# Optimization experiments

Measured on AMD Instinct MI355X. Metric: run time of the kernel, lower is better.

The kernel has to match this reference:

```python
import jax, jax.numpy as jnp
import numpy as np

N_NODES = 50000
N_EDGES = 800000
N_GRAPHS = 2000
N_PAIRS = 4096
IN_CH = 64
EMB = 128
HID = 256
OUT = 1


def gcn_conv(x, edge_index, W, b):
    # PyG GCNConv: h = x @ W^T, then D^{-1/2}(A+I)D^{-1/2} h + b
    h = x @ W.T                                  # [N, out]
    row, col = edge_index[0], edge_index[1]
    ones = jnp.ones((edge_index.shape[1],), h.dtype)
    deg = jax.ops.segment_sum(ones, col, num_segments=N_NODES) + 1.0  # self-loop
    dinv = jax.lax.rsqrt(deg)
    norm = dinv[row] * dinv[col]                 # [E]
    agg = jax.ops.segment_sum(h[row] * norm[:, None], col, num_segments=N_NODES)
    agg = agg + h * (1.0 / deg)[:, None]         # self-loop term (dinv[i]^2)
    return agg + b


def setup_inputs() -> dict:
    key = jax.random.key(0)
    ks = jax.random.split(key, 10)
    x = jax.random.normal(ks[0], (N_NODES, IN_CH), jnp.float32)
    edge_index = jax.random.randint(ks[1], (2, N_EDGES), 0, N_NODES, jnp.int64)
    batch = jnp.sort(jax.random.randint(ks[2], (N_NODES,), 0, N_GRAPHS, jnp.int64))
    drug_drug_batch = jax.random.randint(ks[3], (2, N_PAIRS), 0, N_GRAPHS, jnp.int64)

    def xavier(k, shape):
        fan_out, fan_in = shape
        lim = jnp.sqrt(6.0 / (fan_in + fan_out))
        return jax.random.uniform(k, shape, jnp.float32, -lim, lim)

    return {
        "x": x, "edge_index": edge_index, "batch": batch,
        "drug_drug_batch": drug_drug_batch,
        "conv1_w": xavier(ks[4], (EMB, IN_CH)), "conv1_b": jnp.zeros((EMB,), jnp.float32),
        "conv2_w": xavier(ks[5], (EMB, EMB)), "conv2_b": jnp.zeros((EMB,), jnp.float32),
        "reg1_w": xavier(ks[6], (HID, 2 * EMB)), "reg1_b": jnp.zeros((HID,), jnp.float32),
        "reg2_w": xavier(ks[7], (OUT, HID)), "reg2_b": jnp.zeros((OUT,), jnp.float32),
    }


def reference(x, edge_index, batch, drug_drug_batch,
              conv1_w, conv1_b, conv2_w, conv2_b,
              reg1_w, reg1_b, reg2_w, reg2_b):
    h = jax.nn.relu(gcn_conv(x, edge_index, conv1_w, conv1_b))
    h = jax.nn.relu(gcn_conv(h, edge_index, conv2_w, conv2_b))

    # scatter_mean readout over graphs
    gsum = jax.ops.segment_sum(h, batch, num_segments=N_GRAPHS)
    cnt = jax.ops.segment_sum(jnp.ones((N_NODES,), h.dtype), batch, num_segments=N_GRAPHS)
    graph_embeds = gsum / jnp.maximum(cnt, 1.0)[:, None]

    # quantize drug ids to dense graph indices (np.digitize on unique+1, as in source)
    dd = np.asarray(drug_drug_batch)
    bins = np.unique(dd.flatten()) + 1
    q = jnp.asarray(np.digitize(dd, bins))       # [2, P]

    pairs = jnp.concatenate([graph_embeds[q[0]], graph_embeds[q[1]]], axis=1)  # [P, 2*EMB]
    out = jax.nn.relu(pairs @ reg1_w.T + reg1_b)
    return out @ reg2_w.T + reg2_b
```

## Files before the change

kernel.cpp:

```cpp
#include <hip/hip_runtime.h>

#define N_NODES  50000
#define N_PAD    50048
#define N_EDGES  800000
#define N_GRAPHS 2000
#define N_PAIRS  4096
#define IN_CH    64
#define EMB      128
#define HID      256
#define PPB      16
#define DPAD     16

__global__ void k_zero(float4* __restrict__ p, int n4) {
    int i = blockIdx.x * 256 + threadIdx.x;
    if (i < n4) p[i] = make_float4(0.f, 0.f, 0.f, 0.f);
}

__global__ void k_pre(const int* __restrict__ col, const int* __restrict__ batch,
                      const float* __restrict__ w1, const float* __restrict__ w2,
                      int* __restrict__ deg, int* __restrict__ pos_e, int* __restrict__ cnt,
                      float* __restrict__ wt1, float* __restrict__ wt2) {
    int e = blockIdx.x * 256 + threadIdx.x;
    if (e < N_EDGES) {
        int c = col[e];
        pos_e[e] = atomicAdd(&deg[c * DPAD], 1);
    }
    if (e < N_NODES) atomicAdd(&cnt[batch[e]], 1);
    if (e < EMB * IN_CH) {
        int j = e / IN_CH, k = e % IN_CH;
        wt1[k * EMB + j] = w1[e];
    } else if (e < EMB * IN_CH + EMB * EMB) {
        int t = e - EMB * IN_CH;
        int j = t / EMB, k = t % EMB;
        wt2[k * EMB + j] = w2[t];
    }
}

__device__ inline int wave_incl_scan(int x, int lane) {
    #pragma unroll
    for (int off = 1; off < 64; off <<= 1) {
        int y = __shfl_up(x, off, 64);
        if (lane >= off) x += y;
    }
    return x;
}

__global__ void k_scan1(const int* __restrict__ in, int* __restrict__ part, int n) {
    __shared__ int ws[4];
    int i = blockIdx.x * 256 + threadIdx.x;
    int lane = threadIdx.x & 63, wid = threadIdx.x >> 6;
    int v = (i < n) ? in[i * DPAD] : 0;
    int x = wave_incl_scan(v, lane);
    if (lane == 63) ws[wid] = x;
    __syncthreads();
    if (threadIdx.x == 0) part[blockIdx.x] = ws[0] + ws[1] + ws[2] + ws[3];
}

__global__ void k_scan2d(int* __restrict__ part, int nb,
                         const int* __restrict__ dd, int* __restrict__ rankx) {
    int t = threadIdx.x, lane = t & 63, wid = t >> 6;
    if (blockIdx.x == 0) {
        __shared__ int ws[4];
        int v = (t < nb) ? part[t] : 0;
        int x = wave_incl_scan(v, lane);
        if (lane == 63) ws[wid] = x;
        __syncthreads();
        int add = 0;
        for (int w = 0; w < wid; ++w) add += ws[w];
        if (t < nb) part[t] = x - v + add;
    } else {
        __shared__ int pres[N_GRAPHS];
        __shared__ int ws2[4];
        __shared__ int carry;
        for (int i = t; i < N_GRAPHS; i += 256) pres[i] = 0;
        __syncthreads();
        for (int i = t; i < 2 * N_PAIRS; i += 256) pres[dd[i]] = 1;
        if (t == 0) carry = 0;
        __syncthreads();
        for (int base = 0; base < N_GRAPHS; base += 256) {
            int i = base + t;
            int v = (i < N_GRAPHS) ? pres[i] : 0;
            int x = wave_incl_scan(v, lane);
            if (lane == 63) ws2[wid] = x;
            __syncthreads();
            int add = carry;
            for (int w = 0; w < wid; ++w) add += ws2[w];
            if (i < N_GRAPHS) rankx[i] = x - v + add;
            __syncthreads();
            if (t == 255) carry = add + x;
            __syncthreads();
        }
    }
}

__global__ void k_scan3d(const int* __restrict__ in, const int* __restrict__ part,
                         int* __restrict__ off, float* __restrict__ dinv) {
    __shared__ int ws[4];
    int i = blockIdx.x * 256 + threadIdx.x;
    int lane = threadIdx.x & 63, wid = threadIdx.x >> 6;
    int v = (i < N_NODES) ? in[i * DPAD] : 0;
    int x = wave_incl_scan(v, lane);
    if (lane == 63) ws[wid] = x;
    __syncthreads();
    int add = part[blockIdx.x];
    for (int w = 0; w < wid; ++w) add += ws[w];
    if (i < N_NODES) {
        off[i] = x - v + add;
        dinv[i] = 1.0f / sqrtf((float)(v + 1));
    }
    if (i == 0) off[N_NODES] = N_EDGES;
}

__global__ void k_fill_scale(const int* __restrict__ row, const int* __restrict__ col,
                             const int* __restrict__ pos_e, const int* __restrict__ off,
                             int* __restrict__ csr_row,
                             const float4* __restrict__ x, const float* __restrict__ dinv,
                             float4* __restrict__ xs) {
    int idx = blockIdx.x * 256 + threadIdx.x;
    if (idx < N_EDGES) {
        int c = col[idx];
        int p = pos_e[idx];
        csr_row[off[c] + p] = row[idx];
    } else {
        int i = idx - N_EDGES;
        int n = i >> 4;
        float d = dinv[n];
        float4 v = x[i];
        v.x *= d; v.y *= d; v.z *= d; v.w *= d;
        xs[i] = v;
    }
}

__device__ inline void f4add(float4& a, const float4 b) {
    a.x += b.x; a.y += b.y; a.z += b.z; a.w += b.w;
}

__global__ __launch_bounds__(256) void k_conv1f(
        const float4* __restrict__ xs, const int* __restrict__ csr_row,
        const int* __restrict__ off, const float* __restrict__ dinv,
        const float* __restrict__ w1t, const float* __restrict__ b1,
        float* __restrict__ h1s) {
    __shared__ __align__(16) float a_lds[32 * IN_CH];
    int t = threadIdx.x;
    int base = blockIdx.x * 32;
    {
        int c4 = t & 15;
        #pragma unroll
        for (int g = 0; g < 2; ++g) {
            int nl = (t >> 4) + g * 16;
            int n = base + nl;
            float4 acc = make_float4(0.f, 0.f, 0.f, 0.f);
            if (n < N_NODES) {
                int s = off[n], e = off[n + 1];
                acc = xs[n * 16 + c4];
                int i = s;
                for (; i + 8 <= e; i += 8) {
                    int r0 = csr_row[i + 0], r1 = csr_row[i + 1], r2 = csr_row[i + 2], r3 = csr_row[i + 3];
                    int r4 = csr_row[i + 4], r5 = csr_row[i + 5], r6 = csr_row[i + 6], r7 = csr_row[i + 7];
                    float4 a0 = xs[r0 * 16 + c4], a1 = xs[r1 * 16 + c4];
                    float4 a2 = xs[r2 * 16 + c4], a3 = xs[r3 * 16 + c4];
                    float4 a4 = xs[r4 * 16 + c4], a5 = xs[r5 * 16 + c4];
                    float4 a6 = xs[r6 * 16 + c4], a7 = xs[r7 * 16 + c4];
                    f4add(a0, a1); f4add(a2, a3); f4add(a4, a5); f4add(a6, a7);
                    f4add(a0, a2); f4add(a4, a6);
                    f4add(a0, a4);
                    f4add(acc, a0);
                }
                for (; i < e; ++i) {
                    float4 a = xs[csr_row[i] * 16 + c4];
                    f4add(acc, a);
                }
                float dn = dinv[n];
                acc.x *= dn; acc.y *= dn; acc.z *= dn; acc.w *= dn;
            }
            *reinterpret_cast<float4*>(&a_lds[nl * IN_CH + c4 * 4]) = acc;
        }
    }
    __syncthreads();
    {
        int cq = (t & 31) << 2;
        int rg = t >> 5;
        float4 acc[4];
        #pragma unroll
        for (int r = 0; r < 4; ++r) acc[r] = make_float4(0.f, 0.f, 0.f, 0.f);
        #pragma unroll 2
        for (int k = 0; k < IN_CH; k += 4) {
            float4 w0 = *reinterpret_cast<const float4*>(&w1t[(k + 0) * EMB + cq]);
            float4 w1 = *reinterpret_cast<const float4*>(&w1t[(k + 1) * EMB + cq]);
            float4 w2 = *reinterpret_cast<const float4*>(&w1t[(k + 2) * EMB + cq]);
            float4 w3 = *reinterpret_cast<const float4*>(&w1t[(k + 3) * EMB + cq]);
            #pragma unroll
            for (int r = 0; r < 4; ++r) {
                float4 a = *reinterpret_cast<const float4*>(&a_lds[(rg * 4 + r) * IN_CH + k]);
                acc[r].x = fmaf(a.x, w0.x, fmaf(a.y, w1.x, fmaf(a.z, w2.x, fmaf(a.w, w3.x, acc[r].x))));
                acc[r].y = fmaf(a.x, w0.y, fmaf(a.y, w1.y, fmaf(a.z, w2.y, fmaf(a.w, w3.y, acc[r].y))));
                acc[r].z = fmaf(a.x, w0.z, fmaf(a.y, w1.z, fmaf(a.z, w2.z, fmaf(a.w, w3.z, acc[r].z))));
                acc[r].w = fmaf(a.x, w0.w, fmaf(a.y, w1.w, fmaf(a.z, w2.w, fmaf(a.w, w3.w, acc[r].w))));
            }
        }
        float4 bv = *reinterpret_cast<const float4*>(&b1[cq]);
        #pragma unroll
        for (int r = 0; r < 4; ++r) {
            int row = base + rg * 4 + r;
            if (row < N_NODES) {
                float4 v = acc[r];
                v.x += bv.x; v.y += bv.y; v.z += bv.z; v.w += bv.w;
                float sc = dinv[row];
                v.x = fmaxf(v.x, 0.f) * sc; v.y = fmaxf(v.y, 0.f) * sc;
                v.z = fmaxf(v.z, 0.f) * sc; v.w = fmaxf(v.w, 0.f) * sc;
                *reinterpret_cast<float4*>(&h1s[(size_t)row * EMB + cq]) = v;
            }
        }
    }
}

template <int K>
__global__ void k_gemmv5(const float* __restrict__ A, const float* __restrict__ Wt,
                         float* __restrict__ out) {
    __shared__ __align__(16) float a_lds[64 * K];
    int t = threadIdx.x;
    {
        const float4* Ag = reinterpret_cast<const float4*>(A + (size_t)blockIdx.x * 64 * K);
        float4* Al = reinterpret_cast<float4*>(a_lds);
        constexpr int NV = (64 * K) / (4 * 256);
        #pragma unroll
        for (int i = 0; i < NV; ++i) Al[t + i * 256] = Ag[t + i * 256];
    }
    __syncthreads();
    int cq = (t & 31) << 2;
    int rg = t >> 5;
    float4 acc[8];
    #pragma unroll
    for (int r = 0; r < 8; ++r) acc[r] = make_float4(0.f, 0.f, 0.f, 0.f);
    #pragma unroll 2
    for (int k = 0; k < K; k += 4) {
        float4 w0 = *reinterpret_cast<const float4*>(&Wt[(k + 0) * EMB + cq]);
        float4 w1 = *reinterpret_cast<const float4*>(&Wt[(k + 1) * EMB + cq]);
        float4 w2 = *reinterpret_cast<const float4*>(&Wt[(k + 2) * EMB + cq]);
        float4 w3 = *reinterpret_cast<const float4*>(&Wt[(k + 3) * EMB + cq]);
        #pragma unroll
        for (int r = 0; r < 8; ++r) {
            float4 a = *reinterpret_cast<const float4*>(&a_lds[(rg * 8 + r) * K + k]);
            acc[r].x = fmaf(a.x, w0.x, fmaf(a.y, w1.x, fmaf(a.z, w2.x, fmaf(a.w, w3.x, acc[r].x))));
            acc[r].y = fmaf(a.x, w0.y, fmaf(a.y, w1.y, fmaf(a.z, w2.y, fmaf(a.w, w3.y, acc[r].y))));
            acc[r].z = fmaf(a.x, w0.z, fmaf(a.y, w1.z, fmaf(a.z, w2.z, fmaf(a.w, w3.z, acc[r].z))));
            acc[r].w = fmaf(a.x, w0.w, fmaf(a.y, w1.w, fmaf(a.z, w2.w, fmaf(a.w, w3.w, acc[r].w))));
        }
    }
    int row0 = blockIdx.x * 64 + rg * 8;
    #pragma unroll
    for (int r = 0; r < 8; ++r) {
        int row = row0 + r;
        if (row < N_NODES) {
            *reinterpret_cast<float4*>(&out[(size_t)row * EMB + cq]) = acc[r];
        }
    }
}

template <int HALF>
__global__ void k_gro_h(const float4* __restrict__ t2, const int* __restrict__ csr_row,
                        const int* __restrict__ off, const float* __restrict__ dinv,
                        const float* __restrict__ bias, const int* __restrict__ batch,
                        float* __restrict__ gsum) {
    constexpr int NPB = 16;
    __shared__ __align__(16) float hb[NPB][64];
    __shared__ int bg[NPB];
    int t = threadIdx.x;
    int local = t >> 4;
    int c4 = t & 15;
    int n0 = blockIdx.x * NPB;
    int n = n0 + local;
    if (t < NPB) bg[t] = batch[n0 + t];
    int s = off[n], e = off[n + 1];
    const int cidx = HALF * 16 + c4;
    float4 acc = t2[(size_t)n * 32 + cidx];
    int i = s;
    for (; i + 8 <= e; i += 8) {
        int r0 = csr_row[i + 0], r1 = csr_row[i + 1], r2 = csr_row[i + 2], r3 = csr_row[i + 3];
        int r4 = csr_row[i + 4], r5 = csr_row[i + 5], r6 = csr_row[i + 6], r7 = csr_row[i + 7];
        float4 a0 = t2[(size_t)r0 * 32 + cidx], a1 = t2[(size_t)r1 * 32 + cidx];
        float4 a2 = t2[(size_t)r2 * 32 + cidx], a3 = t2[(size_t)r3 * 32 + cidx];
        float4 a4 = t2[(size_t)r4 * 32 + cidx], a5 = t2[(size_t)r5 * 32 + cidx];
        float4 a6 = t2[(size_t)r6 * 32 + cidx], a7 = t2[(size_t)r7 * 32 + cidx];
        f4add(a0, a1); f4add(a2, a3); f4add(a4, a5); f4add(a6, a7);
        f4add(a0, a2); f4add(a4, a6);
        f4add(a0, a4);
        f4add(acc, a0);
    }
    for (; i < e; ++i) {
        float4 a = t2[(size_t)csr_row[i] * 32 + cidx];
        f4add(acc, a);
    }
    float dn = dinv[n];
    float4 b = reinterpret_cast<const float4*>(bias)[cidx];
    acc.x = fmaxf(fmaf(acc.x, dn, b.x), 0.f);
    acc.y = fmaxf(fmaf(acc.y, dn, b.y), 0.f);
    acc.z = fmaxf(fmaf(acc.z, dn, b.z), 0.f);
    acc.w = fmaxf(fmaf(acc.w, dn, b.w), 0.f);
    *reinterpret_cast<float4*>(&hb[local][c4 * 4]) = acc;
    __syncthreads();
    {
        int ch = t & 63, q = t >> 6;
        int j0 = q * 4;
        int g = bg[j0];
        float a = 0.f;
        #pragma unroll
        for (int j = j0; j < j0 + 4; ++j) {
            int gj = bg[j];
            if (gj != g) { atomicAdd(&gsum[g * EMB + HALF * 64 + ch], a); a = 0.f; g = gj; }
            a += hb[j][ch];
        }
        atomicAdd(&gsum[g * EMB + HALF * 64 + ch], a);
    }
}

__global__ void k_mlp16(const float* __restrict__ gemb, const int* __restrict__ cnt,
                        const int* __restrict__ dd, const int* __restrict__ rankx,
                        const float* __restrict__ w1, const float* __restrict__ b1,
                        const float* __restrict__ w2, const float* __restrict__ b2,
                        float* __restrict__ out) {
    __shared__ __align__(16) float pv[PPB][2 * EMB];
    __shared__ float wpart[4][PPB];
    int p0 = blockIdx.x * PPB;
    int t = threadIdx.x;
    int lane = t & 63, wid = t >> 6;
    #pragma unroll
    for (int j = 0; j < PPB; ++j) {
        int p = p0 + j;
        if (t < EMB) {
            int ga = rankx[dd[p]];
            int ca = cnt[ga];
            float ra = 1.0f / (float)(ca > 1 ? ca : 1);
            pv[j][t] = gemb[ga * EMB + t] * ra;
        } else {
            int gb = rankx[dd[N_PAIRS + p]];
            int cb = cnt[gb];
            float rb = 1.0f / (float)(cb > 1 ? cb : 1);
            pv[j][t] = gemb[gb * EMB + (t - EMB)] * rb;
        }
    }
    __syncthreads();
    float acc[PPB];
    float bv = b1[t];
    #pragma unroll
    for (int j = 0; j < PPB; ++j) acc[j] = bv;
    const float4* wrow = reinterpret_cast<const float4*>(&w1[t * 2 * EMB]);
    for (int k = 0; k < (2 * EMB) / 4; ++k) {
        float4 w = wrow[k];
        #pragma unroll
        for (int j = 0; j < PPB; ++j) {
            const float4 xv = *reinterpret_cast<const float4*>(&pv[j][k * 4]);
            acc[j] = fmaf(xv.x, w.x, fmaf(xv.y, w.y, fmaf(xv.z, w.z, fmaf(xv.w, w.w, acc[j]))));
        }
    }
    float w2t = w2[t];
    float contrib[PPB];
    #pragma unroll
    for (int j = 0; j < PPB; ++j) contrib[j] = fmaxf(acc[j], 0.f) * w2t;
    #pragma unroll
    for (int off = 32; off > 0; off >>= 1) {
        #pragma unroll
        for (int j = 0; j < PPB; ++j) contrib[j] += __shfl_down(contrib[j], off, 64);
    }
    if (lane == 0) {
        #pragma unroll
        for (int j = 0; j < PPB; ++j) wpart[wid][j] = contrib[j];
    }
    __syncthreads();
    if (t < PPB) {
        out[p0 + t] = wpart[0][t] + wpart[1][t] + wpart[2][t] + wpart[3][t] + b2[0];
    }
}

extern "C" void kernel_launch(void* const* d_in, const int* in_sizes, int n_in,
                              void* d_out, int out_size, void* d_ws, size_t ws_size,
                              hipStream_t stream) {
    const float* x        = (const float*)d_in[0];
    const int*   ei       = (const int*)d_in[1];
    const int*   batch    = (const int*)d_in[2];
    const int*   dd       = (const int*)d_in[3];
    const float* conv1_w  = (const float*)d_in[4];
    const float* conv1_b  = (const float*)d_in[5];
    const float* conv2_w  = (const float*)d_in[6];
    const float* conv2_b  = (const float*)d_in[7];
    const float* reg1_w   = (const float*)d_in[8];
    const float* reg1_b   = (const float*)d_in[9];
    const float* reg2_w   = (const float*)d_in[10];
    const float* reg2_b   = (const float*)d_in[11];
    float* outp = (float*)d_out;

    const int* ei_row = ei;
    const int* ei_col = ei + N_EDGES;

    char* ws = (char*)d_ws;
    size_t o = 0;
    auto alloc = [&](size_t bytes) -> void* {
        void* p = ws + o;
        o = (o + bytes + 255) & ~(size_t)255;
        return p;
    };
    size_t zero_start = o;
    int*   deg     = (int*)alloc((size_t)N_NODES * DPAD * 4);
    int*   cnt     = (int*)alloc(N_GRAPHS * 4);
    float* gsum    = (float*)alloc(N_GRAPHS * EMB * 4);
    size_t zero_bytes = o - zero_start;
    int*   off     = (int*)alloc((N_NODES + 1) * 4);
    float* dinv    = (float*)alloc(N_NODES * 4);
    int*   part    = (int*)alloc(256 * 4);
    int*   pos_e   = (int*)alloc(N_EDGES * 4);
    int*   csr_row = (int*)alloc(N_EDGES * 4);
    int*   rankx   = (int*)alloc(N_GRAPHS * 4);
    float* Wt1     = (float*)alloc(IN_CH * EMB * 4);
    float* Wt2     = (float*)alloc(EMB * EMB * 4);
    float* h1s     = (float*)alloc((size_t)N_PAD * EMB * 4);
    float* t2      = (float*)alloc((size_t)N_PAD * EMB * 4);
    float* xs      = t2;

    (void)ws_size; (void)in_sizes; (void)n_in; (void)out_size;

    {
        int n4 = (int)(zero_bytes / 16);
        k_zero<<<(n4 + 255) / 256, 256, 0, stream>>>((float4*)(ws + zero_start), n4);
    }

    k_pre<<<N_EDGES / 256, 256, 0, stream>>>(ei_col, batch, conv1_w, conv2_w,
                                             deg, pos_e, cnt, Wt1, Wt2);
    {
        int nb = (N_NODES + 255) / 256;
        k_scan1<<<nb, 256, 0, stream>>>(deg, part, N_NODES);
        k_scan2d<<<2, 256, 0, stream>>>(part, nb, dd, rankx);
        k_scan3d<<<nb, 256, 0, stream>>>(deg, part, off, dinv);
    }
    k_fill_scale<<<(N_EDGES + N_NODES * (IN_CH / 4)) / 256, 256, 0, stream>>>(
        ei_row, ei_col, pos_e, off, csr_row, (const float4*)x, dinv, (float4*)xs);

    k_conv1f<<<N_PAD / 32, 256, 0, stream>>>(
        (const float4*)xs, csr_row, off, dinv, Wt1, conv1_b, h1s);

    k_gemmv5<EMB><<<N_PAD / 64, 256, 0, stream>>>(h1s, Wt2, t2);
    k_gro_h<0><<<N_NODES / 16, 256, 0, stream>>>(
        (const float4*)t2, csr_row, off, dinv, conv2_b, batch, gsum);
    k_gro_h<1><<<N_NODES / 16, 256, 0, stream>>>(
        (const float4*)t2, csr_row, off, dinv, conv2_b, batch, gsum);

    k_mlp16<<<N_PAIRS / PPB, 256, 0, stream>>>(gsum, cnt, dd, rankx,
                                               reg1_w, reg1_b, reg2_w, reg2_b, outp);
}
```

Baseline: 234.9 us.

## Fold scan-block-sums and digitize into other kernels, remap conv1 gather threads

Removes the separate k_scan2d launch. The digitize/rank computation moves into an extra block of the zero kernel, and each k_scan3d block now computes its own prefix over the per-block partial sums with a reduction. In conv1, each node is handled by 8 threads, each covering 2 channel groups, so a thread loads off/dinv once. The goal is fewer launches and less serial dependency, in exchange for redundant partial-sum reads in every scan3d block and longer per-thread gather loops.

```diff
diff --git a/kernel.cpp b/kernel.cpp
--- a/kernel.cpp
+++ b/kernel.cpp
@@ -11,31 +11,6 @@
 #define PPB      16
 #define DPAD     16
 
-__global__ void k_zero(float4* __restrict__ p, int n4) {
-    int i = blockIdx.x * 256 + threadIdx.x;
-    if (i < n4) p[i] = make_float4(0.f, 0.f, 0.f, 0.f);
-}
-
-__global__ void k_pre(const int* __restrict__ col, const int* __restrict__ batch,
-                      const float* __restrict__ w1, const float* __restrict__ w2,
-                      int* __restrict__ deg, int* __restrict__ pos_e, int* __restrict__ cnt,
-                      float* __restrict__ wt1, float* __restrict__ wt2) {
-    int e = blockIdx.x * 256 + threadIdx.x;
-    if (e < N_EDGES) {
-        int c = col[e];
-        pos_e[e] = atomicAdd(&deg[c * DPAD], 1);
-    }
-    if (e < N_NODES) atomicAdd(&cnt[batch[e]], 1);
-    if (e < EMB * IN_CH) {
-        int j = e / IN_CH, k = e % IN_CH;
-        wt1[k * EMB + j] = w1[e];
-    } else if (e < EMB * IN_CH + EMB * EMB) {
-        int t = e - EMB * IN_CH;
-        int j = t / EMB, k = t % EMB;
-        wt2[k * EMB + j] = w2[t];
-    }
-}
-
 __device__ inline int wave_incl_scan(int x, int lane) {
     #pragma unroll
     for (int off = 1; off < 64; off <<= 1) {
@@ -45,29 +20,13 @@
     return x;
 }
 
-__global__ void k_scan1(const int* __restrict__ in, int* __restrict__ part, int n) {
-    __shared__ int ws[4];
-    int i = blockIdx.x * 256 + threadIdx.x;
-    int lane = threadIdx.x & 63, wid = threadIdx.x >> 6;
-    int v = (i < n) ? in[i * DPAD] : 0;
-    int x = wave_incl_scan(v, lane);
-    if (lane == 63) ws[wid] = x;
-    __syncthreads();
-    if (threadIdx.x == 0) part[blockIdx.x] = ws[0] + ws[1] + ws[2] + ws[3];
-}
-
-__global__ void k_scan2d(int* __restrict__ part, int nb,
-                         const int* __restrict__ dd, int* __restrict__ rankx) {
+__global__ void k_zero_dig(float4* __restrict__ p, int n4,
+                           const int* __restrict__ dd, int* __restrict__ rankx) {
+    int nzb = (n4 + 255) >> 8;
     int t = threadIdx.x, lane = t & 63, wid = t >> 6;
-    if (blockIdx.x == 0) {
-        __shared__ int ws[4];
-        int v = (t < nb) ? part[t] : 0;
-        int x = wave_incl_scan(v, lane);
-        if (lane == 63) ws[wid] = x;
-        __syncthreads();
-        int add = 0;
-        for (int w = 0; w < wid; ++w) add += ws[w];
-        if (t < nb) part[t] = x - v + add;
+    if ((int)blockIdx.x < nzb) {
+        int i = blockIdx.x * 256 + t;
+        if (i < n4) p[i] = make_float4(0.f, 0.f, 0.f, 0.f);
     } else {
         __shared__ int pres[N_GRAPHS];
         __shared__ int ws2[4];
@@ -93,16 +52,54 @@
     }
 }
 
+__global__ void k_pre(const int* __restrict__ col, const int* __restrict__ batch,
+                      const float* __restrict__ w1, const float* __restrict__ w2,
+                      int* __restrict__ deg, int* __restrict__ pos_e, int* __restrict__ cnt,
+                      float* __restrict__ wt1, float* __restrict__ wt2) {
+    int e = blockIdx.x * 256 + threadIdx.x;
+    if (e < N_EDGES) {
+        int c = col[e];
+        pos_e[e] = atomicAdd(&deg[c * DPAD], 1);
+    }
+    if (e < N_NODES) atomicAdd(&cnt[batch[e]], 1);
+    if (e < EMB * IN_CH) {
+        int j = e / IN_CH, k = e % IN_CH;
+        wt1[k * EMB + j] = w1[e];
+    } else if (e < EMB * IN_CH + EMB * EMB) {
+        int t = e - EMB * IN_CH;
+        int j = t / EMB, k = t % EMB;
+        wt2[k * EMB + j] = w2[t];
+    }
+}
+
+__global__ void k_scan1(const int* __restrict__ in, int* __restrict__ part, int n) {
+    __shared__ int ws[4];
+    int i = blockIdx.x * 256 + threadIdx.x;
+    int lane = threadIdx.x & 63, wid = threadIdx.x >> 6;
+    int v = (i < n) ? in[i * DPAD] : 0;
+    int x = wave_incl_scan(v, lane);
+    if (lane == 63) ws[wid] = x;
+    __syncthreads();
+    if (threadIdx.x == 0) part[blockIdx.x] = ws[0] + ws[1] + ws[2] + ws[3];
+}
+
 __global__ void k_scan3d(const int* __restrict__ in, const int* __restrict__ part,
                          int* __restrict__ off, float* __restrict__ dinv) {
     __shared__ int ws[4];
-    int i = blockIdx.x * 256 + threadIdx.x;
-    int lane = threadIdx.x & 63, wid = threadIdx.x >> 6;
+    __shared__ int psum[4];
+    int t = threadIdx.x;
+    int lane = t & 63, wid = t >> 6;
+    int pp = 0;
+    for (int w = t; w < (int)blockIdx.x; w += 256) pp += part[w];
+    #pragma unroll
+    for (int o = 32; o > 0; o >>= 1) pp += __shfl_down(pp, o, 64);
+    if (lane == 0) psum[wid] = pp;
+    int i = blockIdx.x * 256 + t;
     int v = (i < N_NODES) ? in[i * DPAD] : 0;
     int x = wave_incl_scan(v, lane);
     if (lane == 63) ws[wid] = x;
     __syncthreads();
-    int add = part[blockIdx.x];
+    int add = psum[0] + psum[1] + psum[2] + psum[3];
     for (int w = 0; w < wid; ++w) add += ws[w];
     if (i < N_NODES) {
         off[i] = x - v + add;
@@ -144,14 +141,17 @@
     int t = threadIdx.x;
     int base = blockIdx.x * 32;
     {
-        int c4 = t & 15;
+        int c4l = t & 7;
+        int nl = t >> 3;
+        int n = base + nl;
+        int s = 0, e = 0;
+        float dn = 0.f;
+        if (n < N_NODES) { s = off[n]; e = off[n + 1]; dn = dinv[n]; }
         #pragma unroll
         for (int g = 0; g < 2; ++g) {
-            int nl = (t >> 4) + g * 16;
-            int n = base + nl;
+            int c4 = c4l + g * 8;
             float4 acc = make_float4(0.f, 0.f, 0.f, 0.f);
             if (n < N_NODES) {
-                int s = off[n], e = off[n + 1];
                 acc = xs[n * 16 + c4];
                 int i = s;
                 for (; i + 8 <= e; i += 8) {
@@ -170,7 +170,6 @@
                     float4 a = xs[csr_row[i] * 16 + c4];
                     f4add(acc, a);
                 }
-                float dn = dinv[n];
                 acc.x *= dn; acc.y *= dn; acc.z *= dn; acc.w *= dn;
             }
             *reinterpret_cast<float4*>(&a_lds[nl * IN_CH + c4 * 4]) = acc;
@@ -420,7 +419,8 @@
 
     {
         int n4 = (int)(zero_bytes / 16);
-        k_zero<<<(n4 + 255) / 256, 256, 0, stream>>>((float4*)(ws + zero_start), n4);
+        int nzb = (n4 + 255) / 256;
+        k_zero_dig<<<nzb + 1, 256, 0, stream>>>((float4*)(ws + zero_start), n4, dd, rankx);
     }
 
     k_pre<<<N_EDGES / 256, 256, 0, stream>>>(ei_col, batch, conv1_w, conv2_w,
@@ -428,7 +428,6 @@
     {
         int nb = (N_NODES + 255) / 256;
         k_scan1<<<nb, 256, 0, stream>>>(deg, part, N_NODES);
-        k_scan2d<<<2, 256, 0, stream>>>(part, nb, dd, rankx);
         k_scan3d<<<nb, 256, 0, stream>>>(deg, part, off, dinv);
     }
     k_fill_scale<<<(N_EDGES + N_NODES * (IN_CH / 4)) / 256, 256, 0, stream>>>(
```

After: 227.2 us. 3.3% less time.
